# Kernel tuning notes

Measured on AMD Instinct MI355X. Metric: run time of the kernel, lower is better.

Reference implementation:

```python
import jax, jax.numpy as jnp
import numpy as np

K, D = 512, 64


def setup_inputs() -> dict:
    key = jax.random.key(0)
    k1, k2 = jax.random.split(key)
    z_e_x = jax.random.normal(k1, (32, 4096, D), dtype=jnp.float32)
    # nn.Embedding weight initialized uniform(-1/K, 1/K)
    codebook = jax.random.uniform(k2, (K, D), dtype=jnp.float32,
                                  minval=-1.0 / K, maxval=1.0 / K)
    return {"z_e_x": z_e_x, "codebook": codebook}


def reference(z_e_x, codebook):
    # vq(): pairwise squared L2 distances to codebook, then argmin.
    d = z_e_x.shape[-1]
    flat = z_e_x.reshape(-1, d)                                   # [N, D]
    # ||z||^2 - 2 z.e + ||e||^2  (addmm form from original vq)
    dists = (jnp.sum(flat * flat, axis=1, keepdims=True)
             - 2.0 * flat @ codebook.T
             + jnp.sum(codebook * codebook, axis=1))              # [N, K]
    indices = jnp.argmin(dists, axis=1)                            # [N]
    # latents: indices reshaped to input shape minus feature dim
    return indices.reshape(z_e_x.shape[:-1])
```

## Files before the change

### kernel.cpp

```cpp
#include <hip/hip_runtime.h>
#include <math.h>

#define K_CODES 512
#define D_DIM   64
#define BM      128
#define NCHUNK  128
#define THREADS 256
#define LSTR    72
#define EPS_GAP 4e-5f

#define WS_CNT_OFF  2048
#define WS_EH_OFF   4096
#define WS_EL_OFF   77824
#define WS_LIST_OFF 151552

typedef __attribute__((ext_vector_type(8))) short short8v;
typedef __attribute__((ext_vector_type(4))) float f32x4;

__device__ __forceinline__ float np_sumsq64(const float* zarr) {
    float L[16];
#pragma unroll
    for (int j = 0; j < 16; ++j)
        L[j] = __fadd_rn(
            __fadd_rn(__fmul_rn(zarr[j],      zarr[j]),
                      __fmul_rn(zarr[j + 16], zarr[j + 16])),
            __fadd_rn(__fmul_rn(zarr[j + 32], zarr[j + 32]),
                      __fmul_rn(zarr[j + 48], zarr[j + 48])));
    float m[8];
#pragma unroll
    for (int j = 0; j < 8; ++j) m[j] = __fadd_rn(L[j], L[j + 8]);
    float n4[4];
#pragma unroll
    for (int j = 0; j < 4; ++j) n4[j] = __fadd_rn(m[j], m[j + 4]);
    return __fadd_rn(__fadd_rn(n4[0], n4[2]), __fadd_rn(n4[1], n4[3]));
}

__device__ __forceinline__ unsigned short f32_bf16_rne(float x) {
    unsigned int u = __float_as_uint(x);
    unsigned int r = (u + 0x7FFFu + ((u >> 16) & 1u)) >> 16;
    return (unsigned short)r;
}
__device__ __forceinline__ float bf16_f32(unsigned short h) {
    return __uint_as_float(((unsigned int)h) << 16);
}
__device__ __forceinline__ void split2(float x, unsigned short& h, unsigned short& l) {
    h = f32_bf16_rne(x);
    l = f32_bf16_rne(x - bf16_f32(h));
}

__global__ __launch_bounds__(256)
void vq_prep_kernel(const float* __restrict__ cb, float* __restrict__ ws,
                    int do_split) {
    int k = blockIdx.x * blockDim.x + threadIdx.x;
    if (k == 0) *reinterpret_cast<int*>((char*)ws + WS_CNT_OFF) = 0;
    if (k >= K_CODES) return;
    float e[D_DIM];
    const float4* p = reinterpret_cast<const float4*>(cb + (size_t)k * D_DIM);
#pragma unroll
    for (int i = 0; i < 16; ++i) {
        float4 v = p[i];
        e[4*i+0]=v.x; e[4*i+1]=v.y; e[4*i+2]=v.z; e[4*i+3]=v.w;
    }
    ws[k] = np_sumsq64(e);
    if (do_split) {
        unsigned short* eh = reinterpret_cast<unsigned short*>((char*)ws + WS_EH_OFF)
                             + (size_t)k * LSTR;
        unsigned short* el = reinterpret_cast<unsigned short*>((char*)ws + WS_EL_OFF)
                             + (size_t)k * LSTR;
#pragma unroll
        for (int i = 0; i < D_DIM; ++i) {
            unsigned short h, l;
            split2(e[i], h, l);
            eh[i] = h; el[i] = l;
        }
#pragma unroll
        for (int i = D_DIM; i < LSTR; ++i) { eh[i] = 0; el[i] = 0; }
    }
}

__global__ __launch_bounds__(256)
void vq_pass1_fast(const float* __restrict__ z,
                   const unsigned short* __restrict__ eh_g,
                   const unsigned short* __restrict__ el_g,
                   const float* __restrict__ norms, int* __restrict__ out,
                   int* __restrict__ cnt, int* __restrict__ list, int cap, int n) {
    __shared__ __align__(16) unsigned short ehS[NCHUNK * LSTR];
    __shared__ __align__(16) unsigned short elS[NCHUNK * LSTR];
    __shared__ float nrmL[NCHUNK];

    const int tid  = threadIdx.x;
    const int l    = tid & 63;
    const int w    = tid >> 6;
    const int j    = l >> 4;
    const int c16  = l & 15;
    const int base = blockIdx.x * BM;

    short8v bzh[2][2], bzl[2][2];
#pragma unroll
    for (int p = 0; p < 2; ++p) {
        int row = base + (2 * w + p) * 16 + c16;
        if (row >= n) row = n - 1;
        const float* zp = z + (size_t)row * D_DIM + j * 8;
#pragma unroll
        for (int h = 0; h < 2; ++h) {
            float4 v0 = *reinterpret_cast<const float4*>(zp + h * 32);
            float4 v1 = *reinterpret_cast<const float4*>(zp + h * 32 + 4);
            unsigned short hh[8], ll[8];
            split2(v0.x, hh[0], ll[0]); split2(v0.y, hh[1], ll[1]);
            split2(v0.z, hh[2], ll[2]); split2(v0.w, hh[3], ll[3]);
            split2(v1.x, hh[4], ll[4]); split2(v1.y, hh[5], ll[5]);
            split2(v1.z, hh[6], ll[6]); split2(v1.w, hh[7], ll[7]);
            short8v th, tl;
#pragma unroll
            for (int i = 0; i < 8; ++i) { th[i] = (short)hh[i]; tl[i] = (short)ll[i]; }
            bzh[p][h] = th; bzl[p][h] = tl;
        }
    }

    float m1[2] = {INFINITY, INFINITY};
    float m2[2] = {INFINITY, INFINITY};
    int   i1[2] = {0, 0};

    for (int c = 0; c < 4; ++c) {
        __syncthreads();
        {
            const char* esrc = (const char*)eh_g + (size_t)c * (NCHUNK * LSTR * 2);
            const char* lsrc = (const char*)el_g + (size_t)c * (NCHUNK * LSTR * 2);
#pragma unroll
            for (int r2 = 0; r2 < 4; ++r2) {
                size_t off = ((size_t)tid + (size_t)r2 * 256) * 16;
                __builtin_amdgcn_global_load_lds(
                    (const __attribute__((address_space(1))) void*)(esrc + off),
                    (__attribute__((address_space(3))) void*)((char*)ehS + off), 16, 0, 0);
                __builtin_amdgcn_global_load_lds(
                    (const __attribute__((address_space(1))) void*)(lsrc + off),
                    (__attribute__((address_space(3))) void*)((char*)elS + off), 16, 0, 0);
            }
            if (tid < 128) {
                size_t off = 16384 + (size_t)tid * 16;
                __builtin_amdgcn_global_load_lds(
                    (const __attribute__((address_space(1))) void*)(esrc + off),
                    (__attribute__((address_space(3))) void*)((char*)ehS + off), 16, 0, 0);
                __builtin_amdgcn_global_load_lds(
                    (const __attribute__((address_space(1))) void*)(lsrc + off),
                    (__attribute__((address_space(3))) void*)((char*)elS + off), 16, 0, 0);
            }
            if (tid < NCHUNK / 4)
                reinterpret_cast<float4*>(nrmL)[tid] =
                    reinterpret_cast<const float4*>(norms)[c * (NCHUNK / 4) + tid];
        }
        __syncthreads();

#pragma unroll
        for (int ct = 0; ct < 8; ++ct) {
            int ar = (ct * 16 + c16) * LSTR + j * 8;
            short8v aeh0 = *reinterpret_cast<const short8v*>(&ehS[ar]);
            short8v aeh1 = *reinterpret_cast<const short8v*>(&ehS[ar + 32]);
            short8v ael0 = *reinterpret_cast<const short8v*>(&elS[ar]);
            short8v ael1 = *reinterpret_cast<const short8v*>(&elS[ar + 32]);
            float4 nr = *reinterpret_cast<const float4*>(&nrmL[ct * 16 + j * 4]);
            float nra[4] = {nr.x, nr.y, nr.z, nr.w};
            int kg0 = c * NCHUNK + ct * 16 + j * 4;
#pragma unroll
            for (int p = 0; p < 2; ++p) {
                f32x4 acc = {0.f, 0.f, 0.f, 0.f};
                acc = __builtin_amdgcn_mfma_f32_16x16x32_bf16(aeh0, bzh[p][0], acc, 0, 0, 0);
                acc = __builtin_amdgcn_mfma_f32_16x16x32_bf16(aeh1, bzh[p][1], acc, 0, 0, 0);
                acc = __builtin_amdgcn_mfma_f32_16x16x32_bf16(aeh0, bzl[p][0], acc, 0, 0, 0);
                acc = __builtin_amdgcn_mfma_f32_16x16x32_bf16(aeh1, bzl[p][1], acc, 0, 0, 0);
                acc = __builtin_amdgcn_mfma_f32_16x16x32_bf16(ael0, bzh[p][0], acc, 0, 0, 0);
                acc = __builtin_amdgcn_mfma_f32_16x16x32_bf16(ael1, bzh[p][1], acc, 0, 0, 0);
#pragma unroll
                for (int r = 0; r < 4; ++r) {
                    float s = fmaf(-2.0f, acc[r], nra[r]);
                    int kg = kg0 + r;
                    bool lt1 = s < m1[p];
                    float nm2 = lt1 ? m1[p] : fminf(s, m2[p]);
                    i1[p] = lt1 ? kg : i1[p];
                    m1[p] = lt1 ? s : m1[p];
                    m2[p] = nm2;
                }
            }
        }
    }

#pragma unroll
    for (int p = 0; p < 2; ++p) {
        float a1 = m1[p], a2 = m2[p]; int ai = i1[p];
#pragma unroll
        for (int off = 16; off <= 32; off <<= 1) {
            float o1 = __shfl_xor(a1, off, 64);
            float o2 = __shfl_xor(a2, off, 64);
            int   oi = __shfl_xor(ai, off, 64);
            float hi = fmaxf(a1, o1);
            bool take = o1 < a1;
            ai = take ? oi : ai;
            a1 = take ? o1 : a1;
            a2 = fminf(hi, fminf(a2, o2));
        }
        int  ptg    = base + (2 * w + p) * 16 + c16;
        bool writer = (j == 0) && (ptg < n);
        bool flag   = writer && (a2 - a1 <= EPS_GAP);
        unsigned long long m = __ballot(flag);
        int abase = 0;
        if (m) {
            int leader = __ffsll(m) - 1;
            if (l == leader) abase = atomicAdd(cnt, __popcll(m));
            abase = __shfl(abase, leader, 64);
        }
        if (writer) {
            int val = ai;
            if (flag) {
                int rank = __popcll(m & ((1ull << l) - 1ull));
                int slot = abase + rank;
                if (slot < cap) list[slot] = ptg;
                else            val |= (int)0x80000000;
            }
            out[ptg] = val;
        }
    }
}

__global__ __launch_bounds__(256)
void vq_pass1_legacy(const float* __restrict__ z, const float* __restrict__ cb,
                     const float* __restrict__ norms, int* __restrict__ out,
                     int* __restrict__ cnt, int* __restrict__ list, int cap, int n) {
    __shared__ unsigned short zhS[BM * LSTR];
    __shared__ unsigned short zlS[BM * LSTR];
    __shared__ unsigned short ehS[NCHUNK * LSTR];
    __shared__ unsigned short elS[NCHUNK * LSTR];
    __shared__ float nrmL[NCHUNK];

    const int tid  = threadIdx.x;
    const int l    = tid & 63;
    const int w    = tid >> 6;
    const int j    = l >> 4;
    const int c16  = l & 15;
    const int base = blockIdx.x * BM;

    const float4* z4 = reinterpret_cast<const float4*>(z);
#pragma unroll
    for (int rep = 0; rep < 8; ++rep) {
        int flat = rep * THREADS + tid;
        int pt   = flat >> 4;
        int dblk = flat & 15;
        int gp = base + pt; if (gp >= n) gp = n - 1;
        float4 v = z4[(size_t)gp * 16 + dblk];
        ushort4 h, lo;
        split2(v.x, h.x, lo.x); split2(v.y, h.y, lo.y);
        split2(v.z, h.z, lo.z); split2(v.w, h.w, lo.w);
        *reinterpret_cast<ushort4*>(&zhS[pt * LSTR + dblk * 4]) = h;
        *reinterpret_cast<ushort4*>(&zlS[pt * LSTR + dblk * 4]) = lo;
    }
    __syncthreads();

    short8v bzh[2][2], bzl[2][2];
#pragma unroll
    for (int p = 0; p < 2; ++p) {
        int pr = ((2 * w + p) * 16 + c16) * LSTR;
#pragma unroll
        for (int h = 0; h < 2; ++h) {
            int off = pr + h * 32 + j * 8;
            bzh[p][h] = *reinterpret_cast<const short8v*>(&zhS[off]);
            bzl[p][h] = *reinterpret_cast<const short8v*>(&zlS[off]);
        }
    }

    float m1[2] = {INFINITY, INFINITY};
    float m2[2] = {INFINITY, INFINITY};
    int   i1[2] = {0, 0};

    for (int c = 0; c < 4; ++c) {
        __syncthreads();
        const float4* cb4 = reinterpret_cast<const float4*>(cb);
#pragma unroll
        for (int rep = 0; rep < 8; ++rep) {
            int flat = rep * THREADS + tid;
            int code = flat >> 4;
            int dblk = flat & 15;
            float4 v = cb4[(size_t)(c * NCHUNK + code) * 16 + dblk];
            ushort4 h, lo;
            split2(v.x, h.x, lo.x); split2(v.y, h.y, lo.y);
            split2(v.z, h.z, lo.z); split2(v.w, h.w, lo.w);
            *reinterpret_cast<ushort4*>(&ehS[code * LSTR + dblk * 4]) = h;
            *reinterpret_cast<ushort4*>(&elS[code * LSTR + dblk * 4]) = lo;
        }
        if (tid < NCHUNK / 4)
            reinterpret_cast<float4*>(nrmL)[tid] =
                reinterpret_cast<const float4*>(norms)[c * (NCHUNK / 4) + tid];
        __syncthreads();

#pragma unroll
        for (int ct = 0; ct < 8; ++ct) {
            int ar = (ct * 16 + c16) * LSTR + j * 8;
            short8v aeh0 = *reinterpret_cast<const short8v*>(&ehS[ar]);
            short8v aeh1 = *reinterpret_cast<const short8v*>(&ehS[ar + 32]);
            short8v ael0 = *reinterpret_cast<const short8v*>(&elS[ar]);
            short8v ael1 = *reinterpret_cast<const short8v*>(&elS[ar + 32]);
            float4 nr = *reinterpret_cast<const float4*>(&nrmL[ct * 16 + j * 4]);
            float nra[4] = {nr.x, nr.y, nr.z, nr.w};
            int kg0 = c * NCHUNK + ct * 16 + j * 4;
#pragma unroll
            for (int p = 0; p < 2; ++p) {
                f32x4 acc = {0.f, 0.f, 0.f, 0.f};
                acc = __builtin_amdgcn_mfma_f32_16x16x32_bf16(aeh0, bzh[p][0], acc, 0, 0, 0);
                acc = __builtin_amdgcn_mfma_f32_16x16x32_bf16(aeh1, bzh[p][1], acc, 0, 0, 0);
                acc = __builtin_amdgcn_mfma_f32_16x16x32_bf16(aeh0, bzl[p][0], acc, 0, 0, 0);
                acc = __builtin_amdgcn_mfma_f32_16x16x32_bf16(aeh1, bzl[p][1], acc, 0, 0, 0);
                acc = __builtin_amdgcn_mfma_f32_16x16x32_bf16(ael0, bzh[p][0], acc, 0, 0, 0);
                acc = __builtin_amdgcn_mfma_f32_16x16x32_bf16(ael1, bzh[p][1], acc, 0, 0, 0);
#pragma unroll
                for (int r = 0; r < 4; ++r) {
                    float s = fmaf(-2.0f, acc[r], nra[r]);
                    int kg = kg0 + r;
                    bool lt1 = s < m1[p];
                    float nm2 = lt1 ? m1[p] : fminf(s, m2[p]);
                    i1[p] = lt1 ? kg : i1[p];
                    m1[p] = lt1 ? s : m1[p];
                    m2[p] = nm2;
                }
            }
        }
    }

#pragma unroll
    for (int p = 0; p < 2; ++p) {
        float a1 = m1[p], a2 = m2[p]; int ai = i1[p];
#pragma unroll
        for (int off = 16; off <= 32; off <<= 1) {
            float o1 = __shfl_xor(a1, off, 64);
            float o2 = __shfl_xor(a2, off, 64);
            int   oi = __shfl_xor(ai, off, 64);
            float hi = fmaxf(a1, o1);
            bool take = o1 < a1;
            ai = take ? oi : ai;
            a1 = take ? o1 : a1;
            a2 = fminf(hi, fminf(a2, o2));
        }
        int  ptg    = base + (2 * w + p) * 16 + c16;
        bool writer = (j == 0) && (ptg < n);
        bool flag   = writer && (a2 - a1 <= EPS_GAP);
        unsigned long long m = __ballot(flag);
        int abase = 0;
        if (m) {
            int leader = __ffsll(m) - 1;
            if (l == leader) abase = atomicAdd(cnt, __popcll(m));
            abase = __shfl(abase, leader, 64);
        }
        if (writer) {
            int val = ai;
            if (flag) {
                int rank = __popcll(m & ((1ull << l) - 1ull));
                int slot = abase + rank;
                if (slot < cap) list[slot] = ptg;
                else            val |= (int)0x80000000;
            }
            out[ptg] = val;
        }
    }
}

__device__ __forceinline__ void vq_rescan_point(
        const float* __restrict__ z, const float* __restrict__ cb,
        const float* __restrict__ norms, int* __restrict__ out,
        int pt, int lane) {
    float zr[D_DIM];
    const float4* zp = reinterpret_cast<const float4*>(z + (size_t)pt * D_DIM);
#pragma unroll
    for (int i = 0; i < 16; ++i) {
        float4 q = zp[i];
        zr[4*i+0]=q.x; zr[4*i+1]=q.y; zr[4*i+2]=q.z; zr[4*i+3]=q.w;
    }
    const float sz = np_sumsq64(zr);
    float best = INFINITY; int bi = 0x7FFFFFFF;
#pragma unroll 1
    for (int r = 0; r < 8; ++r) {
        const float4* e4 = reinterpret_cast<const float4*>(cb) +
                           ((size_t)(lane * 8 + r) << 4);
        float a = 0.f;
#pragma unroll
        for (int g = 0; g < 16; ++g) {
            float4 q = e4[g];
            a = fmaf(zr[4*g+0], q.x, a);
            a = fmaf(zr[4*g+1], q.y, a);
            a = fmaf(zr[4*g+2], q.z, a);
            a = fmaf(zr[4*g+3], q.w, a);
        }
        float s = __fadd_rn(__fsub_rn(sz, __fmul_rn(2.0f, a)),
                            norms[lane * 8 + r]);
        if (s < best) { best = s; bi = lane * 8 + r; }
    }
#pragma unroll
    for (int off = 1; off < 64; off <<= 1) {
        float os = __shfl_xor(best, off, 64);
        int   ok = __shfl_xor(bi, off, 64);
        if (os < best || (os == best && ok < bi)) { best = os; bi = ok; }
    }
    if (lane == 0) out[pt] = bi;
}

__global__ __launch_bounds__(256)
void vq_cleanup_kernel(const float* __restrict__ z, const float* __restrict__ cb,
                       const float* __restrict__ norms,
                       const int* __restrict__ cnt, const int* __restrict__ list,
                       int cap, int* __restrict__ out, int n) {
    const int lane   = threadIdx.x & 63;
    const int wid    = (blockIdx.x * blockDim.x + threadIdx.x) >> 6;
    const int nwaves = (gridDim.x * blockDim.x) >> 6;

    int total = *cnt;
    int lim   = total < cap ? total : cap;
    for (int i = wid; i < lim; i += nwaves)
        vq_rescan_point(z, cb, norms, out, list[i], lane);

    if (total > cap) {
        for (int b = wid * 64; b < n; b += nwaves * 64) {
            int t = b + lane;
            int v = (t < n) ? out[t] : 0;
            unsigned long long m = __ballot(v < 0);
            while (m) {
                int bb = __ffsll(m) - 1;
                m &= m - 1ull;
                vq_rescan_point(z, cb, norms, out, b + bb, lane);
            }
        }
    }
}

extern "C" void kernel_launch(void* const* d_in, const int* in_sizes, int n_in,
                              void* d_out, int out_size, void* d_ws, size_t ws_size,
                              hipStream_t stream) {
    const float* z  = (const float*)d_in[0];
    const float* cb = (const float*)d_in[1];
    int n = in_sizes[0] / D_DIM;
    float* norms = (float*)d_ws;
    int*   cnt   = (int*)((char*)d_ws + WS_CNT_OFF);
    int* out = (int*)d_out;

    bool fast = ws_size >= (size_t)WS_LIST_OFF + 4096;
    vq_prep_kernel<<<(K_CODES + 255) / 256, 256, 0, stream>>>(cb, norms, fast ? 1 : 0);

    if (fast) {
        const unsigned short* eh = (const unsigned short*)((char*)d_ws + WS_EH_OFF);
        const unsigned short* el = (const unsigned short*)((char*)d_ws + WS_EL_OFF);
        int* list = (int*)((char*)d_ws + WS_LIST_OFF);
        int  cap  = (int)((ws_size - WS_LIST_OFF) / 4);
        vq_pass1_fast<<<(n + BM - 1) / BM, THREADS, 0, stream>>>(
            z, eh, el, norms, out, cnt, list, cap, n);
        vq_cleanup_kernel<<<512, 256, 0, stream>>>(z, cb, norms, cnt, list, cap, out, n);
    } else {
        int* list = (int*)d_ws + 513;
        int  cap  = (int)(ws_size / 4) - 513; if (cap < 0) cap = 0;
        vq_pass1_legacy<<<(n + BM - 1) / BM, THREADS, 0, stream>>>(
            z, cb, norms, out, cnt, list, cap, n);
        vq_cleanup_kernel<<<512, 256, 0, stream>>>(z, cb, norms, cnt, list, cap, out, n);
    }
}
```

Baseline: 63.09 us.

## Double-buffer codebook chunks in LDS and double rows per block

The fast pass now prefetches the next 128-code chunk of the split bf16 codebook and its norms into a second LDS buffer while the current chunk feeds the MFMAs. This removes one barrier per chunk and overlaps the global-to-LDS copy with compute. It also raises BM to 256, so each wave handles four 16-row tiles instead of two, reusing every LDS codebook fragment across more points and halving the block count. The cost is double the LDS footprint and more registers per wave, which may lower occupancy. The legacy path is pinned to the old 128-row tile size.

```diff
diff --git a/kernel.cpp b/kernel.cpp
--- a/kernel.cpp
+++ b/kernel.cpp
@@ -3,7 +3,7 @@
 
 #define K_CODES 512
 #define D_DIM   64
-#define BM      128
+#define BM      256
 #define NCHUNK  128
 #define THREADS 256
 #define LSTR    72
@@ -84,9 +84,9 @@
                    const unsigned short* __restrict__ el_g,
                    const float* __restrict__ norms, int* __restrict__ out,
                    int* __restrict__ cnt, int* __restrict__ list, int cap, int n) {
-    __shared__ __align__(16) unsigned short ehS[NCHUNK * LSTR];
-    __shared__ __align__(16) unsigned short elS[NCHUNK * LSTR];
-    __shared__ float nrmL[NCHUNK];
+    __shared__ __align__(16) unsigned short ehS[2][NCHUNK * LSTR];
+    __shared__ __align__(16) unsigned short elS[2][NCHUNK * LSTR];
+    __shared__ float nrmL[2][NCHUNK];
 
     const int tid  = threadIdx.x;
     const int l    = tid & 63;
@@ -95,10 +95,37 @@
     const int c16  = l & 15;
     const int base = blockIdx.x * BM;
 
-    short8v bzh[2][2], bzl[2][2];
-#pragma unroll
-    for (int p = 0; p < 2; ++p) {
-        int row = base + (2 * w + p) * 16 + c16;
+    {
+        const char* esrc = (const char*)eh_g;
+        const char* lsrc = (const char*)el_g;
+#pragma unroll
+        for (int r2 = 0; r2 < 4; ++r2) {
+            size_t off = ((size_t)tid + (size_t)r2 * 256) * 16;
+            __builtin_amdgcn_global_load_lds(
+                (const __attribute__((address_space(1))) void*)(esrc + off),
+                (__attribute__((address_space(3))) void*)((char*)ehS[0] + off), 16, 0, 0);
+            __builtin_amdgcn_global_load_lds(
+                (const __attribute__((address_space(1))) void*)(lsrc + off),
+                (__attribute__((address_space(3))) void*)((char*)elS[0] + off), 16, 0, 0);
+        }
+        if (tid < 128) {
+            size_t off = 16384 + (size_t)tid * 16;
+            __builtin_amdgcn_global_load_lds(
+                (const __attribute__((address_space(1))) void*)(esrc + off),
+                (__attribute__((address_space(3))) void*)((char*)ehS[0] + off), 16, 0, 0);
+            __builtin_amdgcn_global_load_lds(
+                (const __attribute__((address_space(1))) void*)(lsrc + off),
+                (__attribute__((address_space(3))) void*)((char*)elS[0] + off), 16, 0, 0);
+        }
+        if (tid < NCHUNK / 4)
+            reinterpret_cast<float4*>(nrmL[0])[tid] =
+                reinterpret_cast<const float4*>(norms)[tid];
+    }
+
+    short8v bzh[4][2], bzl[4][2];
+#pragma unroll
+    for (int p = 0; p < 4; ++p) {
+        int row = base + (4 * w + p) * 16 + c16;
         if (row >= n) row = n - 1;
         const float* zp = z + (size_t)row * D_DIM + j * 8;
 #pragma unroll
@@ -117,52 +144,53 @@
         }
     }
 
-    float m1[2] = {INFINITY, INFINITY};
-    float m2[2] = {INFINITY, INFINITY};
-    int   i1[2] = {0, 0};
+    float m1[4] = {INFINITY, INFINITY, INFINITY, INFINITY};
+    float m2[4] = {INFINITY, INFINITY, INFINITY, INFINITY};
+    int   i1[4] = {0, 0, 0, 0};
 
     for (int c = 0; c < 4; ++c) {
+        const int buf = c & 1;
         __syncthreads();
-        {
-            const char* esrc = (const char*)eh_g + (size_t)c * (NCHUNK * LSTR * 2);
-            const char* lsrc = (const char*)el_g + (size_t)c * (NCHUNK * LSTR * 2);
+
+        if (c < 3) {
+            const char* esrc = (const char*)eh_g + (size_t)(c + 1) * (NCHUNK * LSTR * 2);
+            const char* lsrc = (const char*)el_g + (size_t)(c + 1) * (NCHUNK * LSTR * 2);
 #pragma unroll
             for (int r2 = 0; r2 < 4; ++r2) {
                 size_t off = ((size_t)tid + (size_t)r2 * 256) * 16;
                 __builtin_amdgcn_global_load_lds(
                     (const __attribute__((address_space(1))) void*)(esrc + off),
-                    (__attribute__((address_space(3))) void*)((char*)ehS + off), 16, 0, 0);
+                    (__attribute__((address_space(3))) void*)((char*)ehS[buf ^ 1] + off), 16, 0, 0);
                 __builtin_amdgcn_global_load_lds(
                     (const __attribute__((address_space(1))) void*)(lsrc + off),
-                    (__attribute__((address_space(3))) void*)((char*)elS + off), 16, 0, 0);
+                    (__attribute__((address_space(3))) void*)((char*)elS[buf ^ 1] + off), 16, 0, 0);
             }
             if (tid < 128) {
                 size_t off = 16384 + (size_t)tid * 16;
                 __builtin_amdgcn_global_load_lds(
                     (const __attribute__((address_space(1))) void*)(esrc + off),
-                    (__attribute__((address_space(3))) void*)((char*)ehS + off), 16, 0, 0);
+                    (__attribute__((address_space(3))) void*)((char*)ehS[buf ^ 1] + off), 16, 0, 0);
                 __builtin_amdgcn_global_load_lds(
                     (const __attribute__((address_space(1))) void*)(lsrc + off),
-                    (__attribute__((address_space(3))) void*)((char*)elS + off), 16, 0, 0);
+                    (__attribute__((address_space(3))) void*)((char*)elS[buf ^ 1] + off), 16, 0, 0);
             }
             if (tid < NCHUNK / 4)
-                reinterpret_cast<float4*>(nrmL)[tid] =
-                    reinterpret_cast<const float4*>(norms)[c * (NCHUNK / 4) + tid];
-        }
-        __syncthreads();
+                reinterpret_cast<float4*>(nrmL[buf ^ 1])[tid] =
+                    reinterpret_cast<const float4*>(norms)[(c + 1) * (NCHUNK / 4) + tid];
+        }
 
 #pragma unroll
         for (int ct = 0; ct < 8; ++ct) {
             int ar = (ct * 16 + c16) * LSTR + j * 8;
-            short8v aeh0 = *reinterpret_cast<const short8v*>(&ehS[ar]);
-            short8v aeh1 = *reinterpret_cast<const short8v*>(&ehS[ar + 32]);
-            short8v ael0 = *reinterpret_cast<const short8v*>(&elS[ar]);
-            short8v ael1 = *reinterpret_cast<const short8v*>(&elS[ar + 32]);
-            float4 nr = *reinterpret_cast<const float4*>(&nrmL[ct * 16 + j * 4]);
+            short8v aeh0 = *reinterpret_cast<const short8v*>(&ehS[buf][ar]);
+            short8v aeh1 = *reinterpret_cast<const short8v*>(&ehS[buf][ar + 32]);
+            short8v ael0 = *reinterpret_cast<const short8v*>(&elS[buf][ar]);
+            short8v ael1 = *reinterpret_cast<const short8v*>(&elS[buf][ar + 32]);
+            float4 nr = *reinterpret_cast<const float4*>(&nrmL[buf][ct * 16 + j * 4]);
             float nra[4] = {nr.x, nr.y, nr.z, nr.w};
             int kg0 = c * NCHUNK + ct * 16 + j * 4;
 #pragma unroll
-            for (int p = 0; p < 2; ++p) {
+            for (int p = 0; p < 4; ++p) {
                 f32x4 acc = {0.f, 0.f, 0.f, 0.f};
                 acc = __builtin_amdgcn_mfma_f32_16x16x32_bf16(aeh0, bzh[p][0], acc, 0, 0, 0);
                 acc = __builtin_amdgcn_mfma_f32_16x16x32_bf16(aeh1, bzh[p][1], acc, 0, 0, 0);
@@ -185,7 +213,7 @@
     }
 
 #pragma unroll
-    for (int p = 0; p < 2; ++p) {
+    for (int p = 0; p < 4; ++p) {
         float a1 = m1[p], a2 = m2[p]; int ai = i1[p];
 #pragma unroll
         for (int off = 16; off <= 32; off <<= 1) {
@@ -198,7 +226,7 @@
             a1 = take ? o1 : a1;
             a2 = fminf(hi, fminf(a2, o2));
         }
-        int  ptg    = base + (2 * w + p) * 16 + c16;
+        int  ptg    = base + (4 * w + p) * 16 + c16;
         bool writer = (j == 0) && (ptg < n);
         bool flag   = writer && (a2 - a1 <= EPS_GAP);
         unsigned long long m = __ballot(flag);
@@ -225,8 +253,8 @@
 void vq_pass1_legacy(const float* __restrict__ z, const float* __restrict__ cb,
                      const float* __restrict__ norms, int* __restrict__ out,
                      int* __restrict__ cnt, int* __restrict__ list, int cap, int n) {
-    __shared__ unsigned short zhS[BM * LSTR];
-    __shared__ unsigned short zlS[BM * LSTR];
+    __shared__ unsigned short zhS[128 * LSTR];
+    __shared__ unsigned short zlS[128 * LSTR];
     __shared__ unsigned short ehS[NCHUNK * LSTR];
     __shared__ unsigned short elS[NCHUNK * LSTR];
     __shared__ float nrmL[NCHUNK];
@@ -236,7 +264,7 @@
     const int w    = tid >> 6;
     const int j    = l >> 4;
     const int c16  = l & 15;
-    const int base = blockIdx.x * BM;
+    const int base = blockIdx.x * 128;
 
     const float4* z4 = reinterpret_cast<const float4*>(z);
 #pragma unroll
@@ -451,7 +479,7 @@
     } else {
         int* list = (int*)d_ws + 513;
         int  cap  = (int)(ws_size / 4) - 513; if (cap < 0) cap = 0;
-        vq_pass1_legacy<<<(n + BM - 1) / BM, THREADS, 0, stream>>>(
+        vq_pass1_legacy<<<(n + 127) / 128, THREADS, 0, stream>>>(
             z, cb, norms, out, cnt, list, cap, n);
         vq_cleanup_kernel<<<512, 256, 0, stream>>>(z, cb, norms, cnt, list, cap, out, n);
     }
```

Result: slower. 66.08 us (+4.7%).
